# Kernel optimization log

Measured on AMD Instinct MI355X. Metric: run time of the kernel, lower is better.

The kernel has to match this reference:

```python
import jax, jax.numpy as jnp
import numpy as np

B, S, H, D = 4, 2048, 12, 64
WINDOW = 128          # local_attention window => (w//2, w//2) sliding window
BASE = 16000.0        # rope theta (ProkBert default)
NEG = -1e9


def rotate_half(x):
    x1, x2 = jnp.split(x, 2, axis=-1)
    return jnp.concatenate([-x2, x1], axis=-1)


def setup_inputs() -> dict:
    key = jax.random.key(0)
    k1, = jax.random.split(key, 1)
    qkv = jax.random.normal(k1, (B, S, 3, H, D), dtype=jnp.float32)
    pos = jnp.arange(S)
    inv_freq = 1.0 / (BASE ** (jnp.arange(0, D, 2).astype(jnp.float32) / D))
    freqs = pos[:, None].astype(jnp.float32) * inv_freq[None, :]   # (S, D/2)
    emb = jnp.concatenate([freqs, freqs], axis=-1)                  # (S, D)
    cos = jnp.cos(emb)
    sin = jnp.sin(emb)
    dist = jnp.abs(pos[:, None] - pos[None, :])
    mask = jnp.where(dist <= WINDOW // 2, 0.0, NEG).astype(jnp.float32)[None, None]  # (1,1,S,S)
    return {"qkv": qkv, "cos": cos, "sin": sin, "mask": mask}


def reference(qkv, cos, sin, mask):
    # qkv: (B, S, 3, H, D) -> q/k/v: (B, H, S, D)
    q = jnp.swapaxes(qkv[:, :, 0], 1, 2)
    k = jnp.swapaxes(qkv[:, :, 1], 1, 2)
    v = jnp.swapaxes(qkv[:, :, 2], 1, 2)
    cos_b = cos[None, None]   # (1,1,S,D)
    sin_b = sin[None, None]
    q = q * cos_b + rotate_half(q) * sin_b
    k = k * cos_b + rotate_half(k) * sin_b
    scale = D ** -0.5
    scores = jnp.einsum('bhqd,bhkd->bhqk', q, k) * scale + mask
    w = jax.nn.softmax(scores.astype(jnp.float32), axis=-1).astype(q.dtype)
    out = jnp.einsum('bhqk,bhkd->bhqd', w, v)
    out = jnp.swapaxes(out, 1, 2).reshape(B, S, H * D)  # (B, S, dim)
    return out
```

## Files before the change

kernel.cpp:

```cpp
#include <hip/hip_runtime.h>
#include <hip/hip_bf16.h>
#include <cstdint>


typedef short bf16x8 __attribute__((ext_vector_type(8)));
typedef float f32x4  __attribute__((ext_vector_type(4)));
typedef uint32_t u32x4 __attribute__((ext_vector_type(4)));

#define SLEN   2048
#define NHEAD  12
#define NBATCH 4
#define HD     64
#define WHALF  64
#define QT     128
#define KROWS  256
#define NKC    9
#define VST    68
#define VROWS  136
#define QSCALE 0.18033688011112042f


__device__ __forceinline__ short f2b(float f) {
    uint32_t x = __builtin_bit_cast(uint32_t, f);
    x += 0x7FFFu + ((x >> 16) & 1u);
    return (short)(x >> 16);
}
__device__ __forceinline__ uint32_t f2b_pk(float lo, float hi) {
    return (uint32_t)(uint16_t)f2b(lo) | ((uint32_t)(uint16_t)f2b(hi) << 16);
}

__global__ __launch_bounds__(512, 4) void prokbert_attn(
        const float* __restrict__ qkv, const float* __restrict__ cosT,
        const float* __restrict__ sinT, float* __restrict__ out)
{
    __shared__ __align__(16) short    sK[KROWS * 64];
    __shared__ __align__(16) uint32_t sV2[VROWS * VST];

    const int tid = threadIdx.x;

    const int bid = blockIdx.x;
    const int gid = (bid & 7) * 96 + (bid >> 3);
    const int qt = gid & 15;
    const int hh = gid >> 4;
    const int h = hh % NHEAD, b = hh / NHEAD;

    const int q0 = qt * QT;
    const int kstart = q0 - WHALF;

    if (tid < 136) {
        const u32x4 z = {0, 0, 0, 0};
        *(u32x4*)&sV2[128 * VST + tid * 4] = z;
    }

    {
        const int vkp = tid >> 2, vdb = tid & 3, vd0 = vdb * 16;
        const int s0 = kstart + 2 * vkp, s1 = s0 + 1;
        f32x4 va[4], vbv[4];
        const f32x4 z = {0.f, 0.f, 0.f, 0.f};
        if ((unsigned)s0 < SLEN) {
            const f32x4* g0 = (const f32x4*)(qkv +
                (((size_t)(b * SLEN + s0) * 3 + 2) * NHEAD + h) * HD + vd0);
            va[0] = g0[0]; va[1] = g0[1]; va[2] = g0[2]; va[3] = g0[3];
        } else { va[0] = z; va[1] = z; va[2] = z; va[3] = z; }
        if ((unsigned)s1 < SLEN) {
            const f32x4* g1 = (const f32x4*)(qkv +
                (((size_t)(b * SLEN + s1) * 3 + 2) * NHEAD + h) * HD + vd0);
            vbv[0] = g1[0]; vbv[1] = g1[1]; vbv[2] = g1[2]; vbv[3] = g1[3];
        } else { vbv[0] = z; vbv[1] = z; vbv[2] = z; vbv[3] = z; }
        #pragma unroll
        for (int u = 0; u < 4; ++u) {
            u32x4 dw;
            #pragma unroll
            for (int e = 0; e < 4; ++e) dw[e] = f2b_pk(va[u][e], vbv[u][e]);
            *(u32x4*)&sV2[vkp * VST + vd0 + u * 4] = dw;
        }
    }

    {
        const int rrb = tid >> 2, c4 = tid & 3, d0 = c4 * 8;
        f32x4 xl0[2], xl1[2], xh0[2], xh1[2];
        f32x4 cc0[2], cc1[2], ss0[2], ss1[2];
        #pragma unroll
        for (int it = 0; it < 2; ++it) {
            const int rr = rrb + it * 128;
            const int s = kstart + rr;
            if ((unsigned)s < SLEN) {
                const size_t kbase = (((size_t)(b * SLEN + s) * 3 + 1) * NHEAD + h) * HD;
                const f32x4* gxl = (const f32x4*)(qkv + kbase + d0);
                const f32x4* gxh = (const f32x4*)(qkv + kbase + d0 + 32);
                const f32x4* gc  = (const f32x4*)(cosT + s * HD + d0);
                const f32x4* gs  = (const f32x4*)(sinT + s * HD + d0);
                xl0[it] = gxl[0]; xl1[it] = gxl[1];
                xh0[it] = gxh[0]; xh1[it] = gxh[1];
                cc0[it] = gc[0];  cc1[it] = gc[1];
                ss0[it] = gs[0];  ss1[it] = gs[1];
            } else {
                const f32x4 z = {0.f, 0.f, 0.f, 0.f};
                xl0[it] = z; xl1[it] = z; xh0[it] = z; xh1[it] = z;
                cc0[it] = z; cc1[it] = z; ss0[it] = z; ss1[it] = z;
            }
        }
        #pragma unroll
        for (int it = 0; it < 2; ++it) {
            const int rr = rrb + it * 128;
            bf16x8 klo, khi;
            #pragma unroll
            for (int j = 0; j < 4; ++j) {
                klo[j]     = f2b(xl0[it][j] * cc0[it][j] - xh0[it][j] * ss0[it][j]);
                klo[j + 4] = f2b(xl1[it][j] * cc1[it][j] - xh1[it][j] * ss1[it][j]);
                khi[j]     = f2b(xh0[it][j] * cc0[it][j] + xl0[it][j] * ss0[it][j]);
                khi[j + 4] = f2b(xh1[it][j] * cc1[it][j] + xl1[it][j] * ss1[it][j]);
            }
            const int sw = rr & 7;
            *(bf16x8*)&sK[rr * 64 + ((c4 ^ sw) << 3)]       = klo;
            *(bf16x8*)&sK[rr * 64 + (((c4 + 4) ^ sw) << 3)] = khi;
        }
    }

    const int wv = tid >> 6;
    const int lane = tid & 63;
    const int r = lane & 15, g = lane >> 4;
    const int rx = r & 7;
    const int qrow = q0 + wv * 16 + r;
    bf16x8 qf0, qf1;
    {
        const size_t qb = (((size_t)(b * SLEN + qrow) * 3 + 0) * NHEAD + h) * HD;
        const f32x4* ga  = (const f32x4*)(qkv + qb + g * 8);
        const f32x4* gb  = (const f32x4*)(qkv + qb + 32 + g * 8);
        const f32x4* gc0 = (const f32x4*)(cosT + (size_t)qrow * HD + g * 8);
        const f32x4* gs0 = (const f32x4*)(sinT + (size_t)qrow * HD + g * 8);
        f32x4 a0 = ga[0], a1 = ga[1], b0 = gb[0], b1 = gb[1];
        f32x4 c00 = gc0[0], c01 = gc0[1];
        f32x4 s00 = gs0[0], s01 = gs0[1];
        #pragma unroll
        for (int j = 0; j < 4; ++j) {
            qf0[j]     = f2b((a0[j] * c00[j] - b0[j] * s00[j]) * QSCALE);
            qf0[j + 4] = f2b((a1[j] * c01[j] - b1[j] * s01[j]) * QSCALE);
            qf1[j]     = f2b((b0[j] * c00[j] + a0[j] * s00[j]) * QSCALE);
            qf1[j + 4] = f2b((b1[j] * c01[j] + a1[j] * s01[j]) * QSCALE);
        }
    }
    __syncthreads();

    f32x4 sc[NKC];
    #pragma unroll
    for (int kc = 0; kc < NKC; ++kc) {
        const int row = wv * 16 + kc * 16 + r;
        const bf16x8 ka0 = *(const bf16x8*)&sK[row * 64 + ((g ^ rx) << 3)];
        const bf16x8 ka1 = *(const bf16x8*)&sK[row * 64 + (((g + 4) ^ rx) << 3)];
        f32x4 c = {0.f, 0.f, 0.f, 0.f};
        c = __builtin_amdgcn_mfma_f32_16x16x32_bf16(ka0, qf0, c, 0, 0, 0);
        c = __builtin_amdgcn_mfma_f32_16x16x32_bf16(ka1, qf1, c, 0, 0, 0);
        sc[kc] = c;
    }

    bf16x8 pa[5];
    #pragma unroll
    for (int i = 0; i < 8; ++i) pa[4][i] = 0;
    float sum = 0.f;
    #pragma unroll
    for (int kc = 0; kc < NKC; ++kc) {
        #pragma unroll
        for (int i = 0; i < 4; ++i) {
            const int key = kstart + wv * 16 + kc * 16 + g * 4 + i;
            const bool ok = ((unsigned)key < SLEN) &&
                            ((unsigned)(key - qrow + WHALF) <= 2 * WHALF);
            const float e = ok ? exp2f(sc[kc][i]) : 0.f;
            sum += e;
            pa[kc >> 1][((kc & 1) << 2) + i] = f2b(e);
        }
    }
    sum += __shfl_xor(sum, 16);
    sum += __shfl_xor(sum, 32);
    const float inv = 1.f / sum;

    const uint32_t* vptr = &sV2[(wv * 8 + 2 * g) * VST + r];
    f32x4 oacc[4] = {{0,0,0,0},{0,0,0,0},{0,0,0,0},{0,0,0,0}};
    #pragma unroll
    for (int kb = 0; kb < 5; ++kb) {
        #pragma unroll
        for (int dc = 0; dc < 4; ++dc) {
            const int base = kb * 16 * VST + dc * 16;
            u32x4 w;
            w[0] = vptr[base];
            w[1] = vptr[base + VST];
            w[2] = vptr[base + 8 * VST];
            w[3] = vptr[base + 9 * VST];
            const bf16x8 vb = __builtin_bit_cast(bf16x8, w);
            oacc[dc] = __builtin_amdgcn_mfma_f32_16x16x32_bf16(pa[kb], vb, oacc[dc], 0, 0, 0);
        }
    }

    #pragma unroll
    for (int i = 0; i < 4; ++i) {
        const float iq = __shfl(inv, g * 4 + i);
        const int qg = q0 + wv * 16 + g * 4 + i;
        float* orow = out + (((size_t)(b * SLEN + qg)) * NHEAD + h) * HD + r;
        orow[0]  = oacc[0][i] * iq;
        orow[16] = oacc[1][i] * iq;
        orow[32] = oacc[2][i] * iq;
        orow[48] = oacc[3][i] * iq;
    }
}

extern "C" void kernel_launch(void* const* d_in, const int* in_sizes, int n_in,
                              void* d_out, int out_size, void* d_ws, size_t ws_size,
                              hipStream_t stream) {
    const float* qkv  = (const float*)d_in[0];
    const float* cosT = (const float*)d_in[1];
    const float* sinT = (const float*)d_in[2];
    float* out = (float*)d_out;
    dim3 grid(16 * NHEAD * NBATCH);
    dim3 block(512);
    hipLaunchKernelGGL(prokbert_attn, grid, block, 0, stream, qkv, cosT, sinT, out);
}
```

Baseline: 29.50 us.

## Alias K and V in one shared buffer, use hardware bf16 pack, simplify masking

Shared memory is merged into a single buffer: K is staged first, scores are computed, then V overwrites the same space after a barrier. This cuts LDS per block so more blocks can be resident, and launch bounds are raised to 6 blocks. Software bf16 rounding is replaced with the packed hardware conversion instruction. Per-element key masking is reduced to diagonal checks on the first and last chunks, with out-of-range keys corrected by subtracting a count from the sum. The V load and conversion now run after the QK/softmax phase, which adds a second barrier and moves V's global latency onto the critical path.

```diff
diff --git a/kernel.cpp b/kernel.cpp
--- a/kernel.cpp
+++ b/kernel.cpp
@@ -20,21 +20,18 @@
 #define QSCALE 0.18033688011112042f
 
 
-__device__ __forceinline__ short f2b(float f) {
-    uint32_t x = __builtin_bit_cast(uint32_t, f);
-    x += 0x7FFFu + ((x >> 16) & 1u);
-    return (short)(x >> 16);
+__device__ __forceinline__ uint32_t cvt_pk(float lo, float hi) {
+    uint32_t r;
+    asm("v_cvt_pk_bf16_f32 %0, %1, %2" : "=v"(r) : "v"(lo), "v"(hi));
+    return r;
 }
-__device__ __forceinline__ uint32_t f2b_pk(float lo, float hi) {
-    return (uint32_t)(uint16_t)f2b(lo) | ((uint32_t)(uint16_t)f2b(hi) << 16);
-}
-
-__global__ __launch_bounds__(512, 4) void prokbert_attn(
+
+__global__ __launch_bounds__(512, 6) void prokbert_attn(
         const float* __restrict__ qkv, const float* __restrict__ cosT,
         const float* __restrict__ sinT, float* __restrict__ out)
 {
-    __shared__ __align__(16) short    sK[KROWS * 64];
-    __shared__ __align__(16) uint32_t sV2[VROWS * VST];
+    __shared__ __align__(16) uint32_t sbuf[VROWS * VST];
+    short* sKp = (short*)sbuf;
 
     const int tid = threadIdx.x;
 
@@ -47,15 +44,140 @@
     const int q0 = qt * QT;
     const int kstart = q0 - WHALF;
 
-    if (tid < 136) {
-        const u32x4 z = {0, 0, 0, 0};
-        *(u32x4*)&sV2[128 * VST + tid * 4] = z;
-    }
-
+    const int wv = tid >> 6;
+    const int lane = tid & 63;
+    const int r = lane & 15, g = lane >> 4;
+    const int rx = r & 7;
+    const int qrow = q0 + wv * 16 + r;
+
+    const int rrb = tid >> 2, c4 = tid & 3, d0 = c4 * 8;
+    f32x4 xl0[2], xl1[2], xh0[2], xh1[2];
+    f32x4 cc0[2], cc1[2], ss0[2], ss1[2];
+    #pragma unroll
+    for (int it = 0; it < 2; ++it) {
+        const int rr = rrb + it * 128;
+        const int s = kstart + rr;
+        if ((unsigned)s < SLEN) {
+            const size_t kbase = (((size_t)(b * SLEN + s) * 3 + 1) * NHEAD + h) * HD;
+            const f32x4* gxl = (const f32x4*)(qkv + kbase + d0);
+            const f32x4* gxh = (const f32x4*)(qkv + kbase + d0 + 32);
+            const f32x4* gc  = (const f32x4*)(cosT + s * HD + d0);
+            const f32x4* gs  = (const f32x4*)(sinT + s * HD + d0);
+            xl0[it] = gxl[0]; xl1[it] = gxl[1];
+            xh0[it] = gxh[0]; xh1[it] = gxh[1];
+            cc0[it] = gc[0];  cc1[it] = gc[1];
+            ss0[it] = gs[0];  ss1[it] = gs[1];
+        } else {
+            const f32x4 z = {0.f, 0.f, 0.f, 0.f};
+            xl0[it] = z; xl1[it] = z; xh0[it] = z; xh1[it] = z;
+            cc0[it] = z; cc1[it] = z; ss0[it] = z; ss1[it] = z;
+        }
+    }
+    f32x4 qa0, qa1, qb0, qb1, qc0, qc1, qs0, qs1;
     {
-        const int vkp = tid >> 2, vdb = tid & 3, vd0 = vdb * 16;
-        const int s0 = kstart + 2 * vkp, s1 = s0 + 1;
-        f32x4 va[4], vbv[4];
+        const size_t qb = (((size_t)(b * SLEN + qrow) * 3 + 0) * NHEAD + h) * HD;
+        qa0 = ((const f32x4*)(qkv + qb + g * 8))[0];
+        qa1 = ((const f32x4*)(qkv + qb + g * 8))[1];
+        qb0 = ((const f32x4*)(qkv + qb + 32 + g * 8))[0];
+        qb1 = ((const f32x4*)(qkv + qb + 32 + g * 8))[1];
+        qc0 = ((const f32x4*)(cosT + (size_t)qrow * HD + g * 8))[0];
+        qc1 = ((const f32x4*)(cosT + (size_t)qrow * HD + g * 8))[1];
+        qs0 = ((const f32x4*)(sinT + (size_t)qrow * HD + g * 8))[0];
+        qs1 = ((const f32x4*)(sinT + (size_t)qrow * HD + g * 8))[1];
+    }
+    #pragma unroll
+    for (int it = 0; it < 2; ++it) {
+        const int rr = rrb + it * 128;
+        u32x4 klo, khi;
+        #pragma unroll
+        for (int p = 0; p < 2; ++p) {
+            const f32x4 xa = p ? xl1[it] : xl0[it];
+            const f32x4 xb = p ? xh1[it] : xh0[it];
+            const f32x4 cc = p ? cc1[it] : cc0[it];
+            const f32x4 ss = p ? ss1[it] : ss0[it];
+            klo[2 * p]     = cvt_pk(xa[0] * cc[0] - xb[0] * ss[0],
+                                    xa[1] * cc[1] - xb[1] * ss[1]);
+            klo[2 * p + 1] = cvt_pk(xa[2] * cc[2] - xb[2] * ss[2],
+                                    xa[3] * cc[3] - xb[3] * ss[3]);
+            khi[2 * p]     = cvt_pk(xb[0] * cc[0] + xa[0] * ss[0],
+                                    xb[1] * cc[1] + xa[1] * ss[1]);
+            khi[2 * p + 1] = cvt_pk(xb[2] * cc[2] + xa[2] * ss[2],
+                                    xb[3] * cc[3] + xa[3] * ss[3]);
+        }
+        const int sw = rr & 7;
+        *(u32x4*)&sKp[rr * 64 + ((c4 ^ sw) << 3)]       = klo;
+        *(u32x4*)&sKp[rr * 64 + (((c4 + 4) ^ sw) << 3)] = khi;
+    }
+    bf16x8 qf0, qf1;
+    {
+        u32x4 w0, w1;
+        w0[0] = cvt_pk((qa0[0] * qc0[0] - qb0[0] * qs0[0]) * QSCALE,
+                       (qa0[1] * qc0[1] - qb0[1] * qs0[1]) * QSCALE);
+        w0[1] = cvt_pk((qa0[2] * qc0[2] - qb0[2] * qs0[2]) * QSCALE,
+                       (qa0[3] * qc0[3] - qb0[3] * qs0[3]) * QSCALE);
+        w0[2] = cvt_pk((qa1[0] * qc1[0] - qb1[0] * qs1[0]) * QSCALE,
+                       (qa1[1] * qc1[1] - qb1[1] * qs1[1]) * QSCALE);
+        w0[3] = cvt_pk((qa1[2] * qc1[2] - qb1[2] * qs1[2]) * QSCALE,
+                       (qa1[3] * qc1[3] - qb1[3] * qs1[3]) * QSCALE);
+        w1[0] = cvt_pk((qb0[0] * qc0[0] + qa0[0] * qs0[0]) * QSCALE,
+                       (qb0[1] * qc0[1] + qa0[1] * qs0[1]) * QSCALE);
+        w1[1] = cvt_pk((qb0[2] * qc0[2] + qa0[2] * qs0[2]) * QSCALE,
+                       (qb0[3] * qc0[3] + qa0[3] * qs0[3]) * QSCALE);
+        w1[2] = cvt_pk((qb1[0] * qc1[0] + qa1[0] * qs1[0]) * QSCALE,
+                       (qb1[1] * qc1[1] + qa1[1] * qs1[1]) * QSCALE);
+        w1[3] = cvt_pk((qb1[2] * qc1[2] + qa1[2] * qs1[2]) * QSCALE,
+                       (qb1[3] * qc1[3] + qa1[3] * qs1[3]) * QSCALE);
+        qf0 = __builtin_bit_cast(bf16x8, w0);
+        qf1 = __builtin_bit_cast(bf16x8, w1);
+    }
+    __syncthreads();
+
+    f32x4 sc[NKC];
+    #pragma unroll
+    for (int kc = 0; kc < NKC; ++kc) {
+        const int row = wv * 16 + kc * 16 + r;
+        const bf16x8 ka0 = *(const bf16x8*)&sKp[row * 64 + ((g ^ rx) << 3)];
+        const bf16x8 ka1 = *(const bf16x8*)&sKp[row * 64 + (((g + 4) ^ rx) << 3)];
+        f32x4 c = {0.f, 0.f, 0.f, 0.f};
+        c = __builtin_amdgcn_mfma_f32_16x16x32_bf16(ka0, qf0, c, 0, 0, 0);
+        c = __builtin_amdgcn_mfma_f32_16x16x32_bf16(ka1, qf1, c, 0, 0, 0);
+        sc[kc] = c;
+    }
+
+    const int tg = 4 * g;
+    float sum = 0.f;
+    #pragma unroll
+    for (int kc = 0; kc < NKC; ++kc) {
+        #pragma unroll
+        for (int i = 0; i < 4; ++i) {
+            float e = exp2f(sc[kc][i]);
+            if (kc == 0) e = (tg + i >= r) ? e : 0.f;
+            if (kc == 8) e = (tg + i <= r) ? e : 0.f;
+            sc[kc][i] = e;
+            sum += e;
+        }
+    }
+    sum += __shfl_xor(sum, 16);
+    sum += __shfl_xor(sum, 32);
+    const int oob = max(0, WHALF - qrow) + max(0, qrow - (SLEN - 1 - WHALF));
+    const float inv = 1.f / (sum - (float)oob);
+
+    u32x4 paw[5];
+    #pragma unroll
+    for (int kb = 0; kb < 4; ++kb) {
+        paw[kb][0] = cvt_pk(sc[2 * kb][0], sc[2 * kb][1]);
+        paw[kb][1] = cvt_pk(sc[2 * kb][2], sc[2 * kb][3]);
+        paw[kb][2] = cvt_pk(sc[2 * kb + 1][0], sc[2 * kb + 1][1]);
+        paw[kb][3] = cvt_pk(sc[2 * kb + 1][2], sc[2 * kb + 1][3]);
+    }
+    paw[4][0] = cvt_pk(sc[8][0], sc[8][1]);
+    paw[4][1] = cvt_pk(sc[8][2], sc[8][3]);
+    paw[4][2] = 0; paw[4][3] = 0;
+
+    const int vkp = tid >> 2, vdb = tid & 3, vd0 = vdb * 16;
+    const int s0 = kstart + 2 * vkp, s1 = s0 + 1;
+    f32x4 va[4], vb4[4];
+    {
         const f32x4 z = {0.f, 0.f, 0.f, 0.f};
         if ((unsigned)s0 < SLEN) {
             const f32x4* g0 = (const f32x4*)(qkv +
@@ -65,119 +187,31 @@
         if ((unsigned)s1 < SLEN) {
             const f32x4* g1 = (const f32x4*)(qkv +
                 (((size_t)(b * SLEN + s1) * 3 + 2) * NHEAD + h) * HD + vd0);
-            vbv[0] = g1[0]; vbv[1] = g1[1]; vbv[2] = g1[2]; vbv[3] = g1[3];
-        } else { vbv[0] = z; vbv[1] = z; vbv[2] = z; vbv[3] = z; }
-        #pragma unroll
-        for (int u = 0; u < 4; ++u) {
-            u32x4 dw;
-            #pragma unroll
-            for (int e = 0; e < 4; ++e) dw[e] = f2b_pk(va[u][e], vbv[u][e]);
-            *(u32x4*)&sV2[vkp * VST + vd0 + u * 4] = dw;
-        }
-    }
-
-    {
-        const int rrb = tid >> 2, c4 = tid & 3, d0 = c4 * 8;
-        f32x4 xl0[2], xl1[2], xh0[2], xh1[2];
-        f32x4 cc0[2], cc1[2], ss0[2], ss1[2];
-        #pragma unroll
-        for (int it = 0; it < 2; ++it) {
-            const int rr = rrb + it * 128;
-            const int s = kstart + rr;
-            if ((unsigned)s < SLEN) {
-                const size_t kbase = (((size_t)(b * SLEN + s) * 3 + 1) * NHEAD + h) * HD;
-                const f32x4* gxl = (const f32x4*)(qkv + kbase + d0);
-                const f32x4* gxh = (const f32x4*)(qkv + kbase + d0 + 32);
-                const f32x4* gc  = (const f32x4*)(cosT + s * HD + d0);
-                const f32x4* gs  = (const f32x4*)(sinT + s * HD + d0);
-                xl0[it] = gxl[0]; xl1[it] = gxl[1];
-                xh0[it] = gxh[0]; xh1[it] = gxh[1];
-                cc0[it] = gc[0];  cc1[it] = gc[1];
-                ss0[it] = gs[0];  ss1[it] = gs[1];
-            } else {
-                const f32x4 z = {0.f, 0.f, 0.f, 0.f};
-                xl0[it] = z; xl1[it] = z; xh0[it] = z; xh1[it] = z;
-                cc0[it] = z; cc1[it] = z; ss0[it] = z; ss1[it] = z;
-            }
-        }
-        #pragma unroll
-        for (int it = 0; it < 2; ++it) {
-            const int rr = rrb + it * 128;
-            bf16x8 klo, khi;
-            #pragma unroll
-            for (int j = 0; j < 4; ++j) {
-                klo[j]     = f2b(xl0[it][j] * cc0[it][j] - xh0[it][j] * ss0[it][j]);
-                klo[j + 4] = f2b(xl1[it][j] * cc1[it][j] - xh1[it][j] * ss1[it][j]);
-                khi[j]     = f2b(xh0[it][j] * cc0[it][j] + xl0[it][j] * ss0[it][j]);
-                khi[j + 4] = f2b(xh1[it][j] * cc1[it][j] + xl1[it][j] * ss1[it][j]);
-            }
-            const int sw = rr & 7;
-            *(bf16x8*)&sK[rr * 64 + ((c4 ^ sw) << 3)]       = klo;
-            *(bf16x8*)&sK[rr * 64 + (((c4 + 4) ^ sw) << 3)] = khi;
-        }
-    }
-
-    const int wv = tid >> 6;
-    const int lane = tid & 63;
-    const int r = lane & 15, g = lane >> 4;
-    const int rx = r & 7;
-    const int qrow = q0 + wv * 16 + r;
-    bf16x8 qf0, qf1;
-    {
-        const size_t qb = (((size_t)(b * SLEN + qrow) * 3 + 0) * NHEAD + h) * HD;
-        const f32x4* ga  = (const f32x4*)(qkv + qb + g * 8);
-        const f32x4* gb  = (const f32x4*)(qkv + qb + 32 + g * 8);
-        const f32x4* gc0 = (const f32x4*)(cosT + (size_t)qrow * HD + g * 8);
-        const f32x4* gs0 = (const f32x4*)(sinT + (size_t)qrow * HD + g * 8);
-        f32x4 a0 = ga[0], a1 = ga[1], b0 = gb[0], b1 = gb[1];
-        f32x4 c00 = gc0[0], c01 = gc0[1];
-        f32x4 s00 = gs0[0], s01 = gs0[1];
-        #pragma unroll
-        for (int j = 0; j < 4; ++j) {
-            qf0[j]     = f2b((a0[j] * c00[j] - b0[j] * s00[j]) * QSCALE);
-            qf0[j + 4] = f2b((a1[j] * c01[j] - b1[j] * s01[j]) * QSCALE);
-            qf1[j]     = f2b((b0[j] * c00[j] + a0[j] * s00[j]) * QSCALE);
-            qf1[j + 4] = f2b((b1[j] * c01[j] + a1[j] * s01[j]) * QSCALE);
-        }
+            vb4[0] = g1[0]; vb4[1] = g1[1]; vb4[2] = g1[2]; vb4[3] = g1[3];
+        } else { vb4[0] = z; vb4[1] = z; vb4[2] = z; vb4[3] = z; }
     }
     __syncthreads();
 
-    f32x4 sc[NKC];
-    #pragma unroll
-    for (int kc = 0; kc < NKC; ++kc) {
-        const int row = wv * 16 + kc * 16 + r;
-        const bf16x8 ka0 = *(const bf16x8*)&sK[row * 64 + ((g ^ rx) << 3)];
-        const bf16x8 ka1 = *(const bf16x8*)&sK[row * 64 + (((g + 4) ^ rx) << 3)];
-        f32x4 c = {0.f, 0.f, 0.f, 0.f};
-        c = __builtin_amdgcn_mfma_f32_16x16x32_bf16(ka0, qf0, c, 0, 0, 0);
-        c = __builtin_amdgcn_mfma_f32_16x16x32_bf16(ka1, qf1, c, 0, 0, 0);
-        sc[kc] = c;
-    }
-
-    bf16x8 pa[5];
-    #pragma unroll
-    for (int i = 0; i < 8; ++i) pa[4][i] = 0;
-    float sum = 0.f;
-    #pragma unroll
-    for (int kc = 0; kc < NKC; ++kc) {
-        #pragma unroll
-        for (int i = 0; i < 4; ++i) {
-            const int key = kstart + wv * 16 + kc * 16 + g * 4 + i;
-            const bool ok = ((unsigned)key < SLEN) &&
-                            ((unsigned)(key - qrow + WHALF) <= 2 * WHALF);
-            const float e = ok ? exp2f(sc[kc][i]) : 0.f;
-            sum += e;
-            pa[kc >> 1][((kc & 1) << 2) + i] = f2b(e);
-        }
-    }
-    sum += __shfl_xor(sum, 16);
-    sum += __shfl_xor(sum, 32);
-    const float inv = 1.f / sum;
-
-    const uint32_t* vptr = &sV2[(wv * 8 + 2 * g) * VST + r];
+    #pragma unroll
+    for (int u = 0; u < 4; ++u) {
+        u32x4 dw;
+        dw[0] = cvt_pk(va[u][0], vb4[u][0]);
+        dw[1] = cvt_pk(va[u][1], vb4[u][1]);
+        dw[2] = cvt_pk(va[u][2], vb4[u][2]);
+        dw[3] = cvt_pk(va[u][3], vb4[u][3]);
+        *(u32x4*)&sbuf[vkp * VST + vd0 + u * 4] = dw;
+    }
+    if (tid < 136) {
+        const u32x4 z = {0, 0, 0, 0};
+        *(u32x4*)&sbuf[128 * VST + tid * 4] = z;
+    }
+    __syncthreads();
+
+    const uint32_t* vptr = &sbuf[(wv * 8 + 2 * g) * VST + r];
     f32x4 oacc[4] = {{0,0,0,0},{0,0,0,0},{0,0,0,0},{0,0,0,0}};
     #pragma unroll
     for (int kb = 0; kb < 5; ++kb) {
+        const bf16x8 pa = __builtin_bit_cast(bf16x8, paw[kb]);
         #pragma unroll
         for (int dc = 0; dc < 4; ++dc) {
             const int base = kb * 16 * VST + dc * 16;
@@ -187,7 +221,7 @@
             w[2] = vptr[base + 8 * VST];
             w[3] = vptr[base + 9 * VST];
             const bf16x8 vb = __builtin_bit_cast(bf16x8, w);
-            oacc[dc] = __builtin_amdgcn_mfma_f32_16x16x32_bf16(pa[kb], vb, oacc[dc], 0, 0, 0);
+            oacc[dc] = __builtin_amdgcn_mfma_f32_16x16x32_bf16(pa, vb, oacc[dc], 0, 0, 0);
         }
     }
 
```

Result: faster. 27.26 us (-7.6%).
